# Kernel optimization log

Hardware: AMD Instinct MI355X
Metric: run time of the kernel (lower is better)

Reference implementation:

```python
import jax, jax.numpy as jnp
import numpy as np

EPS = 1e-9
LAMBDA_VIOLATION = 0.5

B, S, K, N, M = 2048, 20, 128, 256, 10  # batch, num_samples, k, n, m


def setup_inputs() -> dict:
    key = jax.random.key(0)
    k1, k2, k3, k4 = jax.random.split(key, 4)
    y_pred = jax.random.uniform(k1, (B, 1), dtype=jnp.float32) * 10.0 + 1.0
    y_true = jax.random.uniform(k2, (B, 1), dtype=jnp.float32) * 10.0 + 1.0
    P_padded = jax.random.normal(k3, (B, K, N - K), dtype=jnp.float32)
    samples = jax.random.normal(k4, (B, S, K), dtype=jnp.float32)
    return {"y_pred": y_pred, "y_true": y_true, "P_padded": P_padded,
            "samples": samples, "m": M}


def reference(y_pred, y_true, P_padded, samples, m):
    b, s, k = samples.shape
    n = k + P_padded.shape[2]
    # LogMSE term
    yp = jnp.clip(y_pred, EPS)
    yt = jnp.clip(y_true, EPS)
    logmse = jnp.mean((jnp.log2(yt) - jnp.log2(yp)) ** 2)
    # Build generator matrices G = [I_k | P] : [B, k, n]
    I = jnp.broadcast_to(jnp.eye(k, dtype=P_padded.dtype), (b, k, k))
    G = jnp.concatenate([I, P_padded], axis=2)
    # Random codewords: [B, S, n]
    codewords = jnp.einsum('bsk,bkn->bsn', samples, G)
    mags = jnp.abs(codewords).reshape(b * s, n)
    top_vals, _ = jax.lax.top_k(mags, m + 1)  # [B*S, m+1] descending
    hm = (top_vals[:, 0] / (top_vals[:, m] + EPS)).reshape(b, s)
    max_hm = jnp.max(hm, axis=1)  # [B]
    penalty = jnp.sum(jax.nn.relu(max_hm - y_pred.squeeze(-1)))
    violation = penalty / b
    total_loss = logmse + LAMBDA_VIOLATION * violation
    return total_loss, logmse, violation
```

## Files before the change

kernel.cpp:

```cpp
#include <hip/hip_runtime.h>
#include <math.h>

#define EPSF 1e-9f
#define KK 128
#define MTOP 10


#define GLDS16(G, L) __builtin_amdgcn_global_load_lds(                    \
    (const __attribute__((address_space(1))) void*)(G),                   \
    (__attribute__((address_space(3))) void*)(L), 16, 0, 0)

#define STAGE_ISSUE(T, BUF, I)                                            \
    GLDS16(Pb + (size_t)(((T) << 3) + rowoff + (wave << 2) + ((I) << 1)   \
                         + l5) * KK + (lx << 2),                          \
           &sP[BUF][((wave << 2) + ((I) << 1)) * KK])
#define STAGE_CHUNK(T, BUF) { STAGE_ISSUE(T, BUF, 0); STAGE_ISSUE(T, BUF, 1); }

#define FMA5G(T, BUF, G)                                                  \
    {                                                                     \
        const float* pbse = &sP[BUF][((sg << 3) + ((G) << 2)) * KK + j4]; \
        float4 p0 = *(const float4*)(pbse + 0 * KK);                      \
        float4 p1 = *(const float4*)(pbse + 1 * KK);                      \
        float4 p2 = *(const float4*)(pbse + 2 * KK);                      \
        float4 p3 = *(const float4*)(pbse + 3 * KK);                      \
        const int soff = kbase + ((T) << 3) + ((G) << 2);                 \
        _Pragma("unroll")                                                 \
        for (int r = 0; r < 5; ++r) {                                     \
            float4 s = *(const float4*)&sS[(r0 + r) * KK + soff];         \
            acc[r].x = fmaf(s.x, p0.x, acc[r].x);                         \
            acc[r].y = fmaf(s.x, p0.y, acc[r].y);                         \
            acc[r].z = fmaf(s.x, p0.z, acc[r].z);                         \
            acc[r].w = fmaf(s.x, p0.w, acc[r].w);                         \
            acc[r].x = fmaf(s.y, p1.x, acc[r].x);                         \
            acc[r].y = fmaf(s.y, p1.y, acc[r].y);                         \
            acc[r].z = fmaf(s.y, p1.z, acc[r].z);                         \
            acc[r].w = fmaf(s.y, p1.w, acc[r].w);                         \
            acc[r].x = fmaf(s.z, p2.x, acc[r].x);                         \
            acc[r].y = fmaf(s.z, p2.y, acc[r].y);                         \
            acc[r].z = fmaf(s.z, p2.z, acc[r].z);                         \
            acc[r].w = fmaf(s.z, p2.w, acc[r].w);                         \
            acc[r].x = fmaf(s.w, p3.x, acc[r].x);                         \
            acc[r].y = fmaf(s.w, p3.y, acc[r].y);                         \
            acc[r].z = fmaf(s.w, p3.z, acc[r].z);                         \
            acc[r].w = fmaf(s.w, p3.w, acc[r].w);                         \
        }                                                                 \
    }

__global__ __launch_bounds__(256, 6) void fused_kernel(
    const float* __restrict__ y_pred, const float* __restrict__ y_true,
    const float* __restrict__ P, const float* __restrict__ samples,
    float* __restrict__ partial )
{
    const int tid   = threadIdx.x;
    const int wave  = tid >> 6;
    const int lane  = tid & 63;
    const int b     = blockIdx.x;
    const int r0    = wave * 5;
    const int sg    = lane >> 5;
    const int c     = lane & 31;
    const int j4    = c << 2;
    const int kbase = sg << 6;
    const int l5    = lane >> 5;
    const int lx    = lane & 31;
    const int rowoff = (wave >= 2) ? 56 : 0;

    const float* __restrict__ Pb = P + ((size_t)b << 14);
    const float* __restrict__ Sb = samples + (size_t)b * (20 * KK);

    __shared__ float sS[20 * KK];
    __shared__ float sP[2][16 * KK];
    __shared__ float red[4];

#pragma unroll
    for (int i = 0; i < 5; ++i) {
        const int idx = (i * 256 + tid) * 2;
        *(float2*)&sS[idx] = *(const float2*)(Sb + idx);
    }

    float4 acc[5];
#pragma unroll
    for (int r = 0; r < 5; ++r) acc[r] = make_float4(0.f, 0.f, 0.f, 0.f);

    STAGE_CHUNK(0, 0);
    __syncthreads();

    int cur = 0;
#pragma unroll 1
    for (int t = 0; t < 7; ++t) {
        STAGE_CHUNK(t + 1, cur ^ 1);
        FMA5G(t, cur, 0)
        FMA5G(t, cur, 1)
        __syncthreads();
        cur ^= 1;
    }
    FMA5G(7, cur, 0)
    FMA5G(7, cur, 1)

    float w0[5], w1[5], w2[5], w3[5];
#pragma unroll
    for (int r = 0; r < 5; ++r) {
        float ax = acc[r].x + __shfl_xor(acc[r].x, 32, 64);
        float ay = acc[r].y + __shfl_xor(acc[r].y, 32, 64);
        float az = acc[r].z + __shfl_xor(acc[r].z, 32, 64);
        float aw = acc[r].w + __shfl_xor(acc[r].w, 32, 64);
        float4 idv = *(const float4*)&sS[(r0 + r) * KK + j4];
        w0[r] = fabsf(sg ? idv.x : ax);
        w1[r] = fabsf(sg ? idv.y : ay);
        w2[r] = fabsf(sg ? idv.z : az);
        w3[r] = fabsf(sg ? idv.w : aw);
    }

    float mx[5];
#pragma unroll
    for (int r = 0; r < 5; ++r) {
        float lm = fmaxf(fmaxf(w0[r], w1[r]), fmaxf(w2[r], w3[r]));
#pragma unroll
        for (int d = 32; d >= 1; d >>= 1)
            lm = fmaxf(lm, __shfl_xor(lm, d, 64));
        mx[r] = lm;
    }

    unsigned lo[5], hi[5];
#pragma unroll
    for (int r = 0; r < 5; ++r) { lo[r] = 0u; hi[r] = __float_as_uint(mx[r]); }

    while (lo[0] < hi[0] || lo[1] < hi[1] || lo[2] < hi[2] ||
           lo[3] < hi[3] || lo[4] < hi[4]) {
#pragma unroll
        for (int r = 0; r < 5; ++r) {
            unsigned mid = lo[r] + ((hi[r] - lo[r] + 1u) >> 1);
            float mf = __uint_as_float(mid);
            int cnt = __popcll(__ballot(w0[r] > mf)) + __popcll(__ballot(w1[r] > mf))
                    + __popcll(__ballot(w2[r] > mf)) + __popcll(__ballot(w3[r] > mf));
            bool g = cnt >= (MTOP + 1);
            lo[r] = g ? mid : lo[r];
            hi[r] = g ? hi[r] : mid - 1u;
        }
    }

    float hmax = 0.f;
#pragma unroll
    for (int r = 0; r < 5; ++r) {
        float m11 = __uint_as_float(lo[r] + 1u);
        hmax = fmaxf(hmax, mx[r] / (m11 + EPSF));
    }

    if (lane == 0) red[wave] = hmax;
    __syncthreads();
    if (tid == 0) {
        float hb  = fmaxf(fmaxf(red[0], red[1]), fmaxf(red[2], red[3]));
        float ypv = y_pred[b];
        float yp  = fmaxf(ypv, EPSF);
        float yt  = fmaxf(y_true[b], EPSF);
        float d   = log2f(yt) - log2f(yp);
        partial[2 * b]     = d * d;
        partial[2 * b + 1] = fmaxf(hb - ypv, 0.f);
    }
}

__global__ __launch_bounds__(256) void finalize_kernel(
    const float* __restrict__ partial, float* __restrict__ out, float invB)
{
    const int t = threadIdx.x;
    float sl = 0.f, sp = 0.f;
#pragma unroll
    for (int i = 0; i < 8; ++i) {
        float2 v = *(const float2*)(partial + 2 * (t + i * 256));
        sl += v.x; sp += v.y;
    }
#pragma unroll
    for (int d = 32; d >= 1; d >>= 1) {
        sl += __shfl_xor(sl, d, 64);
        sp += __shfl_xor(sp, d, 64);
    }
    __shared__ float rl[4], rp[4];
    const int w = t >> 6;
    if ((t & 63) == 0) { rl[w] = sl; rp[w] = sp; }
    __syncthreads();
    if (t == 0) {
        float L = (rl[0] + rl[1] + rl[2] + rl[3]) * invB;
        float V = (rp[0] + rp[1] + rp[2] + rp[3]) * invB;
        out[0] = L + 0.5f * V;
        out[1] = L;
        out[2] = V;
    }
}

extern "C" void kernel_launch(void* const* d_in, const int* in_sizes, int n_in,
                              void* d_out, int out_size, void* d_ws, size_t ws_size,
                              hipStream_t stream) {
    const float* y_pred  = (const float*)d_in[0];
    const float* y_true  = (const float*)d_in[1];
    const float* P       = (const float*)d_in[2];
    const float* samples = (const float*)d_in[3];
    const int B = in_sizes[0];

    float* partial = (float*)d_ws;

    fused_kernel<<<B, 256, 0, stream>>>(y_pred, y_true, P, samples, partial);
    finalize_kernel<<<1, 256, 0, stream>>>(partial, (float*)d_out, 1.0f / (float)B);
}
```

Baseline: 232.1 us.

## Deepen P staging to a 5-buffer ring with vmcnt-based async waits

Replaces the double-buffered 16-row P staging with a 5-slot ring of 8-row chunks, keeping several global-to-LDS loads in flight. Waits on vmcnt counts and uses raw s_barrier with sched barriers in place of __syncthreads, so only the needed loads must finish before each step. The goal is to hide global memory latency better in this bandwidth-bound batched GEMV. In exchange LDS use grows, launch bounds drop to 4 blocks per CU, and correctness now depends on hand-counted waitcnt values and the ring-slot reuse order.

Measured after the change: 234.9 us. No clear change (+1.2%).

```diff
diff --git a/kernel.cpp b/kernel.cpp
--- a/kernel.cpp
+++ b/kernel.cpp
@@ -10,23 +10,24 @@
     (const __attribute__((address_space(1))) void*)(G),                   \
     (__attribute__((address_space(3))) void*)(L), 16, 0, 0)
 
-#define STAGE_ISSUE(T, BUF, I)                                            \
-    GLDS16(Pb + (size_t)(((T) << 3) + rowoff + (wave << 2) + ((I) << 1)   \
-                         + l5) * KK + (lx << 2),                          \
-           &sP[BUF][((wave << 2) + ((I) << 1)) * KK])
-#define STAGE_CHUNK(T, BUF) { STAGE_ISSUE(T, BUF, 0); STAGE_ISSUE(T, BUF, 1); }
-
-#define FMA5G(T, BUF, G)                                                  \
+#define STAGE(T, BUF)                                                     \
+    GLDS16(Pb + (size_t)(((T) << 2) + ((wave & 1) << 1) +                 \
+                         ((wave >> 1) << 6) + l5) * KK + (lx << 2),       \
+           &sP[(BUF) * (8 * KK) + (((wave & 1) << 1) +                    \
+                                   ((wave >> 1) << 2)) * KK])
+
+#define COMPUTE(T, BUF)                                                   \
     {                                                                     \
-        const float* pbse = &sP[BUF][((sg << 3) + ((G) << 2)) * KK + j4]; \
-        float4 p0 = *(const float4*)(pbse + 0 * KK);                      \
-        float4 p1 = *(const float4*)(pbse + 1 * KK);                      \
-        float4 p2 = *(const float4*)(pbse + 2 * KK);                      \
-        float4 p3 = *(const float4*)(pbse + 3 * KK);                      \
-        const int soff = kbase + ((T) << 3) + ((G) << 2);                 \
+        const float* __restrict__ pb =                                    \
+            &sP[(BUF) * (8 * KK) + (sg << 2) * KK + j4];                  \
+        float4 p0 = *(const float4*)(pb + 0 * KK);                        \
+        float4 p1 = *(const float4*)(pb + 1 * KK);                        \
+        float4 p2 = *(const float4*)(pb + 2 * KK);                        \
+        float4 p3 = *(const float4*)(pb + 3 * KK);                        \
+        const int kk = (T) << 2;                                          \
         _Pragma("unroll")                                                 \
         for (int r = 0; r < 5; ++r) {                                     \
-            float4 s = *(const float4*)&sS[(r0 + r) * KK + soff];         \
+            float4 s = *(const float4*)&sS[(r0 + r) * KK + kbase + kk];   \
             acc[r].x = fmaf(s.x, p0.x, acc[r].x);                         \
             acc[r].y = fmaf(s.x, p0.y, acc[r].y);                         \
             acc[r].z = fmaf(s.x, p0.z, acc[r].z);                         \
@@ -46,7 +47,17 @@
         }                                                                 \
     }
 
-__global__ __launch_bounds__(256, 6) void fused_kernel(
+#define SBAR()                                                            \
+    __builtin_amdgcn_sched_barrier(0);                                    \
+    __builtin_amdgcn_s_barrier();                                         \
+    __builtin_amdgcn_sched_barrier(0)
+
+#define TAILSTEP(T, WAITASM)                                              \
+    asm volatile(WAITASM ::: "memory");                                   \
+    SBAR();                                                               \
+    COMPUTE(T, (T) % 5)
+
+__global__ __launch_bounds__(256, 4) void fused_kernel(
     const float* __restrict__ y_pred, const float* __restrict__ y_true,
     const float* __restrict__ P, const float* __restrict__ samples,
     float* __restrict__ partial )
@@ -62,13 +73,12 @@
     const int kbase = sg << 6;
     const int l5    = lane >> 5;
     const int lx    = lane & 31;
-    const int rowoff = (wave >= 2) ? 56 : 0;
 
     const float* __restrict__ Pb = P + ((size_t)b << 14);
     const float* __restrict__ Sb = samples + (size_t)b * (20 * KK);
 
+    __shared__ float sP[5 * 8 * KK];
     __shared__ float sS[20 * KK];
-    __shared__ float sP[2][16 * KK];
     __shared__ float red[4];
 
 #pragma unroll
@@ -81,20 +91,23 @@
 #pragma unroll
     for (int r = 0; r < 5; ++r) acc[r] = make_float4(0.f, 0.f, 0.f, 0.f);
 
-    STAGE_CHUNK(0, 0);
-    __syncthreads();
-
-    int cur = 0;
+    STAGE(0, 0); STAGE(1, 1); STAGE(2, 2); STAGE(3, 3);
+    asm volatile("s_waitcnt lgkmcnt(0)" ::: "memory");
+    __builtin_amdgcn_sched_barrier(0);
+
 #pragma unroll 1
-    for (int t = 0; t < 7; ++t) {
-        STAGE_CHUNK(t + 1, cur ^ 1);
-        FMA5G(t, cur, 0)
-        FMA5G(t, cur, 1)
-        __syncthreads();
-        cur ^= 1;
-    }
-    FMA5G(7, cur, 0)
-    FMA5G(7, cur, 1)
+    for (int t = 0; t < 12; ++t) {
+        asm volatile("s_waitcnt vmcnt(3)" ::: "memory");
+        SBAR();
+        const int cb = t % 5;
+        COMPUTE(t, cb);
+        const int nb = (t + 4) % 5;
+        STAGE(t + 4, nb);
+    }
+    TAILSTEP(12, "s_waitcnt vmcnt(3)");
+    TAILSTEP(13, "s_waitcnt vmcnt(2)");
+    TAILSTEP(14, "s_waitcnt vmcnt(1)");
+    TAILSTEP(15, "s_waitcnt vmcnt(0)");
 
     float w0[5], w1[5], w2[5], w3[5];
 #pragma unroll
```
